# Kernel tuning notes

Hardware: AMD Instinct MI355X
Metric: run time of the kernel (lower is better)

The kernel has to match this reference:

```python
import jax, jax.numpy as jnp
import numpy as np

D_MODEL = 1024
NHEAD = 16
HEAD_DIM = D_MODEL // NHEAD
SF_THRESHOLD = 4.0
SF_LEVELS = 8
SF_STEP = SF_THRESHOLD / SF_LEVELS  # 0.5
EPS = 1e-6


def sfn(x):
    # Scale-and-Fire neuron: quantize activations to multiples of SF_STEP,
    # clipped to +/- num_levels, with straight-through estimator.
    q = jnp.clip(jnp.round(x / SF_STEP), -SF_LEVELS, SF_LEVELS) * SF_STEP
    return x + jax.lax.stop_gradient(q - x)


def qk_norm(x, g):
    # RMS-normalize over the head_dim (last axis) with learnable gain g [Dh].
    rms = jnp.sqrt(jnp.mean(x * x, axis=-1, keepdims=True) + EPS)
    return (x / rms) * g


def setup_inputs() -> dict:
    key = jax.random.key(0)
    ks = jax.random.split(key, 10)
    B, L, D = 2, 2048, D_MODEL
    s = 1.0 / np.sqrt(D)
    return {
        "x": jax.random.normal(ks[0], (B, L, D), dtype=jnp.float32),
        "Wq": jax.random.normal(ks[1], (D, D), dtype=jnp.float32) * s,
        "bq": jnp.zeros((D,), dtype=jnp.float32),
        "Wk": jax.random.normal(ks[2], (D, D), dtype=jnp.float32) * s,
        "bk": jnp.zeros((D,), dtype=jnp.float32),
        "Wv": jax.random.normal(ks[3], (D, D), dtype=jnp.float32) * s,
        "bv": jnp.zeros((D,), dtype=jnp.float32),
        "Wo": jax.random.normal(ks[4], (D, D), dtype=jnp.float32) * s,
        "bo": jnp.zeros((D,), dtype=jnp.float32),
        "gq": jnp.ones((HEAD_DIM,), dtype=jnp.float32),
        "gk": jnp.ones((HEAD_DIM,), dtype=jnp.float32),
    }


def reference(x, Wq, bq, Wk, bk, Wv, bv, Wo, bo, gq, gk):
    B, L, D = x.shape
    H, Dh = NHEAD, HEAD_DIM
    scale = Dh ** (-0.5)

    q = sfn(x @ Wq.T + bq)
    k = sfn(x @ Wk.T + bk)
    v = sfn(x @ Wv.T + bv)

    # [B, L, H, Dh] -> [B, H, L, Dh]
    q = q.reshape(B, L, H, Dh).transpose(0, 2, 1, 3)
    k = k.reshape(B, L, H, Dh).transpose(0, 2, 1, 3)
    v = v.reshape(B, L, H, Dh).transpose(0, 2, 1, 3)

    q = qk_norm(q, gq)
    k = qk_norm(k, gk)

    scores = jnp.einsum('bhqd,bhkd->bhqk', q, k) * scale
    probs = jax.nn.softmax(scores, axis=-1)  # dropout is identity (eval)
    out = jnp.einsum('bhqk,bhkd->bhqd', probs, v)
    out = out.transpose(0, 2, 1, 3).reshape(B, L, D)
    return out @ Wo.T + bo
```

## Files before the change

### kernel.cpp

```cpp
#include <hip/hip_runtime.h>
#include <math.h>


typedef __bf16 bf16;
typedef bf16 bf16x4 __attribute__((ext_vector_type(4)));
typedef bf16 bf16x8 __attribute__((ext_vector_type(8)));
typedef float f32x4 __attribute__((ext_vector_type(4)));
typedef float f32x16 __attribute__((ext_vector_type(16)));
typedef unsigned int u32;
typedef u32 u32x4 __attribute__((ext_vector_type(4)));

#define LOG2E 1.4426950408889634f
#define MFMA16 __builtin_amdgcn_mfma_f32_16x16x32_bf16
#define MFMA32 __builtin_amdgcn_mfma_f32_32x32x16_bf16
#define S_WAITV(N) asm volatile("s_waitcnt vmcnt(" #N ")" ::: "memory")

__device__ __forceinline__ void bar() {
  asm volatile("" ::: "memory");
  __builtin_amdgcn_s_barrier();
  asm volatile("" ::: "memory");
}

__device__ __forceinline__ float sfn_f(float x) {
  return fminf(fmaxf(rintf(x + x), -8.0f), 8.0f) * 0.5f;
}

__device__ __forceinline__ void gload16(const bf16* g, bf16* l) {
  __builtin_amdgcn_global_load_lds((const __attribute__((address_space(1))) void*)g,
                                   (__attribute__((address_space(3))) void*)l, 16, 0, 0);
}

__device__ __forceinline__ u32 pkbf16(float a, float b) {
  unsigned short ua = __builtin_bit_cast(unsigned short, (bf16)a);
  unsigned short ub = __builtin_bit_cast(unsigned short, (bf16)b);
  return (u32)ua | ((u32)ub << 16);
}


__global__ __launch_bounds__(256) void prep_x_kernel(const float* __restrict__ x,
                                                     bf16* __restrict__ ax) {
  int idx = blockIdx.x * 256 + threadIdx.x;
  int m  = idx >> 8;
  int kc = (idx & 255) << 2;
  const float4 v = *(const float4*)(x + (size_t)m * 1024 + kc);
  bf16 h0 = (bf16)v.x, h1 = (bf16)v.y, h2 = (bf16)v.z, h3 = (bf16)v.w;
  bf16 l0 = (bf16)(v.x - (float)h0), l1 = (bf16)(v.y - (float)h1),
       l2 = (bf16)(v.z - (float)h2), l3 = (bf16)(v.w - (float)h3);
  bf16x4 hv = {h0, h1, h2, h3};
  bf16x4 lv = {l0, l1, l2, l3};
  bf16* p = ax + (size_t)m * 3072 + kc;
  *(bf16x4*)(p)        = hv;
  *(bf16x4*)(p + 1024) = lv;
  *(bf16x4*)(p + 2048) = hv;
}

__global__ __launch_bounds__(256) void prep_w_kernel(const float* __restrict__ Wq,
                                                     const float* __restrict__ Wk,
                                                     const float* __restrict__ Wv,
                                                     bf16* __restrict__ wc) {
  int idx = blockIdx.x * 256 + threadIdx.x;
  int mat = idx >> 18;
  int r   = idx & 262143;
  int n   = r >> 8;
  int kc  = (r & 255) << 2;
  const float* W = (mat == 0) ? Wq : ((mat == 1) ? Wk : Wv);
  const float4 v = *(const float4*)(W + (size_t)n * 1024 + kc);
  bf16 h0 = (bf16)v.x, h1 = (bf16)v.y, h2 = (bf16)v.z, h3 = (bf16)v.w;
  bf16 l0 = (bf16)(v.x - (float)h0), l1 = (bf16)(v.y - (float)h1),
       l2 = (bf16)(v.z - (float)h2), l3 = (bf16)(v.w - (float)h3);
  bf16x4 hv = {h0, h1, h2, h3};
  bf16x4 lv = {l0, l1, l2, l3};
  bf16* p = wc + (size_t)(mat * 1024 + n) * 3072 + kc;
  *(bf16x4*)(p)        = hv;
  *(bf16x4*)(p + 1024) = hv;
  *(bf16x4*)(p + 2048) = lv;
}

__global__ __launch_bounds__(256) void prep_wo_kernel(const float* __restrict__ Wo,
                                                      bf16* __restrict__ wob) {
  int idx = blockIdx.x * 256 + threadIdx.x;
  const float4 v = *(const float4*)(Wo + (size_t)idx * 4);
  bf16x4 hv = {(bf16)v.x, (bf16)v.y, (bf16)v.z, (bf16)v.w};
  *(bf16x4*)(wob + (size_t)idx * 4) = hv;
}


__global__ __launch_bounds__(512, 2) void gemm_qkv_kernel(
    const bf16* __restrict__ A, const bf16* __restrict__ Bm,
    const float* __restrict__ b0, const float* __restrict__ b1,
    const float* __restrict__ b2, const float* __restrict__ g0,
    const float* __restrict__ g1, bf16* __restrict__ qn, bf16* __restrict__ kn,
    bf16* __restrict__ vt) {
  constexpr int K = 3072, NT = 48;
  __shared__ bf16 lds[2][28672];
  const int tid  = threadIdx.x;
  const int wave = tid >> 6;
  const int lane = tid & 63;
  const int lm   = lane & 15;
  const int kg   = lane >> 4;
  const int lid     = blockIdx.x;
  const int logical = ((lid & 7) << 5) | (lid >> 3);
  const int m0 = (logical >> 4) << 8;
  const int n0 = (logical & 15) * 192;

  auto stageA = [&](int buf, int half, int kt) {
#pragma unroll
    for (int j = 0; j < 2; ++j) {
      const int c    = j * 512 + tid;
      const int row  = c >> 3;
      const int col8 = (c & 7) ^ (row & 7);
      gload16(A + (size_t)(m0 + half * 128 + row) * K + kt + col8 * 8,
              &lds[buf][half * 8192 + c * 8]);
    }
  };
  auto stageB = [&](int buf, int ch, int kt) {
    const int row  = tid >> 3;
    const int col8 = (tid & 7) ^ (row & 7);
    gload16(Bm + (size_t)(n0 + ch * 64 + row) * K + kt + col8 * 8,
            &lds[buf][16384 + ch * 4096 + tid * 8]);
  };

  const int sw    = lm & 7;
  const int arow  = (wave << 5) + lm;
  auto rdA = [&](int buf, int r, int kk) -> bf16x8 {
    const int row = arow + 16 * r;
    return *(const bf16x8*)&lds[buf][(row >> 7) * 8192 + (row & 127) * 64 +
                                     (((kk << 2) + kg) ^ sw) * 8];
  };
  auto rdB = [&](int buf, int c, int kk) -> bf16x8 {
    const int col = 16 * c + lm;
    return *(const bf16x8*)&lds[buf][16384 + (col >> 6) * 4096 + (col & 63) * 64 +
                                     (((kk << 2) + kg) ^ sw) * 8];
  };

  f32x4 acc[2][12] = {};

  stageA(0, 0, 0); stageA(0, 1, 0);
  stageB(0, 0, 0); stageB(0, 1, 0); stageB(0, 2, 0);
  stageA(1, 0, 64); stageA(1, 1, 64);
  S_WAITV(4);
  bar();

  for (int t = 0; t < NT; ++t) {
    const int cur = t & 1, nxt = cur ^ 1;
    const int kt1 = (t + 1) << 6, kt2 = (t + 2) << 6;
    bf16x8 a[2][2], bv[6];
#pragma unroll
    for (int r = 0; r < 2; ++r)
#pragma unroll
      for (int kk = 0; kk < 2; ++kk)
        a[r][kk] = rdA(cur, r, kk);
#pragma unroll
    for (int c = 0; c < 6; ++c) bv[c] = rdB(cur, c, 0);
    if (t + 1 < NT) stageB(nxt, 0, kt1);
    bar();
    __builtin_amdgcn_s_setprio(1);
#pragma unroll
    for (int r = 0; r < 2; ++r)
#pragma unroll
      for (int c = 0; c < 6; ++c)
        acc[r][c] = MFMA16(a[r][0], bv[c], acc[r][c], 0, 0, 0);
    __builtin_amdgcn_s_setprio(0);
    bar();
    bf16x8 bw[6];
#pragma unroll
    for (int c = 0; c < 6; ++c) bw[c] = rdB(cur, c + 6, 0);
    if (t + 1 < NT) { stageB(nxt, 1, kt1); stageB(nxt, 2, kt1); }
    bar();
    __builtin_amdgcn_s_setprio(1);
#pragma unroll
    for (int r = 0; r < 2; ++r)
#pragma unroll
      for (int c = 0; c < 6; ++c)
        acc[r][c + 6] = MFMA16(a[r][0], bw[c], acc[r][c + 6], 0, 0, 0);
    __builtin_amdgcn_s_setprio(0);
    bar();
    bf16x8 bx[6];
#pragma unroll
    for (int c = 0; c < 6; ++c) bx[c] = rdB(cur, c, 1);
    bar();
    __builtin_amdgcn_s_setprio(1);
#pragma unroll
    for (int r = 0; r < 2; ++r)
#pragma unroll
      for (int c = 0; c < 6; ++c)
        acc[r][c] = MFMA16(a[r][1], bx[c], acc[r][c], 0, 0, 0);
    __builtin_amdgcn_s_setprio(0);
    bar();
    bf16x8 by[6];
#pragma unroll
    for (int c = 0; c < 6; ++c) by[c] = rdB(cur, c + 6, 1);
    if (t + 2 < NT) {
      stageA(cur, 0, kt2); stageA(cur, 1, kt2);
      S_WAITV(4);
    } else {
      S_WAITV(0);
    }
    bar();
    __builtin_amdgcn_s_setprio(1);
#pragma unroll
    for (int r = 0; r < 2; ++r)
#pragma unroll
      for (int c = 0; c < 6; ++c)
        acc[r][c + 6] = MFMA16(a[r][1], by[c], acc[r][c + 6], 0, 0, 0);
    __builtin_amdgcn_s_setprio(0);
    bar();
  }

#pragma unroll
  for (int h = 0; h < 3; ++h) {
    const int gcol = n0 + (h << 6);
    const int mat  = gcol >> 10;
    const int cb   = gcol & 1023;
    const int hh   = cb >> 6;
    const float* bias = (mat == 0) ? b0 : ((mat == 1) ? b1 : b2);
    float bvals[4];
#pragma unroll
    for (int j = 0; j < 4; ++j) bvals[j] = bias[cb + 16 * j + lm];

    if (mat < 2) {
      const float* gain = (mat == 0) ? g0 : g1;
      bf16* dst = (mat == 0) ? qn : kn;
      float gv[4];
#pragma unroll
      for (int j = 0; j < 4; ++j) gv[j] = gain[16 * j + lm];
#pragma unroll
      for (int r = 0; r < 2; ++r) {
        float y[4][4];
        float ss[4] = {0.f, 0.f, 0.f, 0.f};
#pragma unroll
        for (int j = 0; j < 4; ++j)
#pragma unroll
          for (int g = 0; g < 4; ++g) {
            float tq = sfn_f(acc[r][4 * h + j][g] + bvals[j]);
            y[j][g] = tq;
            ss[g] += tq * tq;
          }
#pragma unroll
        for (int g = 0; g < 4; ++g) {
          float s = ss[g];
          s += __shfl_xor(s, 1);
          s += __shfl_xor(s, 2);
          s += __shfl_xor(s, 4);
          s += __shfl_xor(s, 8);
          ss[g] = 1.0f / sqrtf(s * (1.0f / 64.0f) + 1e-6f);
        }
        const int mbase = m0 + (wave << 5) + 16 * r + 4 * kg;
        const int bb = mbase >> 11;
        const int ll = mbase & 2047;
#pragma unroll
        for (int g = 0; g < 4; ++g) {
          bf16* rowp = dst + ((size_t)(bb * 16 + hh) * 2048 + (ll + g)) * 64;
#pragma unroll
          for (int j = 0; j < 4; ++j)
            rowp[16 * j + lm] = (bf16)(y[j][g] * ss[g] * gv[j]);
        }
      }
    } else {
#pragma unroll
      for (int r = 0; r < 2; ++r) {
        const int mbase = m0 + (wave << 5) + 16 * r + 4 * kg;
        const int bb = mbase >> 11;
        const int ll = mbase & 2047;
#pragma unroll
        for (int j = 0; j < 4; ++j) {
          bf16x4 pk;
#pragma unroll
          for (int g = 0; g < 4; ++g)
            pk[g] = (bf16)sfn_f(acc[r][4 * h + j][g] + bvals[j]);
          *(bf16x4*)(vt + ((size_t)(bb * 16 + hh) * 64 + 16 * j + lm) * 2048 + ll) = pk;
        }
      }
    }
  }
}


__global__ __launch_bounds__(256, 3) void gemm_o_kernel(
    const bf16* __restrict__ A, const bf16* __restrict__ Bm, int K,
    const float* __restrict__ b0, float* __restrict__ outf) {
  __shared__ bf16 sA[128 * 32];
  __shared__ bf16 sB[128 * 32];
  const int tid  = threadIdx.x;
  const int wave = tid >> 6;
  const int lane = tid & 63;
  const int lm   = lane & 15;
  const int kg   = lane >> 4;
  const int nbx = gridDim.x;
  const int lid = blockIdx.x + nbx * blockIdx.y;
  const int cpx = (nbx << 5) >> 3;
  const int logical = (lid & 7) * cpx + (lid >> 3);
  const int m0 = (logical / nbx) << 7;
  const int n0 = (logical % nbx) << 7;
  const int wm = (wave >> 1) << 6;
  const int wn = (wave & 1) << 6;

  f32x4 acc[4][4] = {};

  for (int kt = 0; kt < K; kt += 32) {
    __syncthreads();
#pragma unroll
    for (int j = 0; j < 2; ++j) {
      const int i   = wave * 128 + j * 64 + lane;
      const int row = i >> 2;
      const int kc  = (i & 3) << 3;
      gload16(A  + (size_t)(m0 + row) * K + kt + kc, sA + i * 8);
      gload16(Bm + (size_t)(n0 + row) * K + kt + kc, sB + i * 8);
    }
    __syncthreads();
    bf16x8 af[4], bfv[4];
#pragma unroll
    for (int r = 0; r < 4; ++r)
      af[r] = *(const bf16x8*)(sA + (wm + 16 * r + lm) * 32 + kg * 8);
#pragma unroll
    for (int c = 0; c < 4; ++c)
      bfv[c] = *(const bf16x8*)(sB + (wn + 16 * c + lm) * 32 + kg * 8);
#pragma unroll
    for (int r = 0; r < 4; ++r)
#pragma unroll
      for (int c = 0; c < 4; ++c)
        acc[r][c] = MFMA16(af[r], bfv[c], acc[r][c], 0, 0, 0);
  }

  float bvals[4];
#pragma unroll
  for (int c = 0; c < 4; ++c) bvals[c] = b0[n0 + wn + 16 * c + lm];
#pragma unroll
  for (int r = 0; r < 4; ++r) {
    const int mr = m0 + wm + 16 * r + 4 * kg;
#pragma unroll
    for (int c = 0; c < 4; ++c) {
      const int nc = n0 + wn + 16 * c + lm;
#pragma unroll
      for (int g = 0; g < 4; ++g)
        outf[(size_t)(mr + g) * 1024 + nc] = acc[r][c][g] + bvals[c];
    }
  }
}


__global__ __launch_bounds__(256, 2) void attn_kernel(const bf16* __restrict__ qn,
                                                      const bf16* __restrict__ kn,
                                                      const bf16* __restrict__ vt,
                                                      bf16* __restrict__ ao) {
  __shared__ bf16 sK[2][64 * 64];
  __shared__ bf16 sV[2][64 * 64];
  const int tid  = threadIdx.x;
  const int wave = tid >> 6;
  const int lane = tid & 63;
  const int l31  = lane & 31;
  const int hi   = lane >> 5;
  const int lid     = blockIdx.x + (blockIdx.y << 4);
  const int logical = ((lid & 7) << 6) | (lid >> 3);
  const int qblk    = logical & 15;
  const int bh      = logical >> 4;
  const int q0      = (qblk << 7) + (wave << 5);
  const bf16* qb = qn + (size_t)bh * 2048 * 64;
  const bf16* kb = kn + (size_t)bh * 2048 * 64;
  const bf16* vb = vt + (size_t)bh * 64 * 2048;

  const float C1 = 0.125f * LOG2E;
  const float C2 = -8.0f * LOG2E;

  const int srow7 = lane >> 3;
  const int scl   = (lane & 7) ^ srow7;
  auto stageK = [&](int buf, int kt) {
#pragma unroll
    for (int j = 0; j < 2; ++j) {
      const int ci  = wave * 2 + j;
      const int row = ci * 8 + srow7;
      gload16(kb + (size_t)(kt + row) * 64 + scl * 8, &sK[buf][ci * 512]);
    }
  };
  auto stageV = [&](int buf, int kt) {
#pragma unroll
    for (int j = 0; j < 2; ++j) {
      const int ci  = wave * 2 + j;
      const int row = ci * 8 + srow7;
      gload16(vb + (size_t)row * 2048 + kt + scl * 8, &sV[buf][ci * 512]);
    }
  };

  bf16x8 qf[4];
#pragma unroll
  for (int j = 0; j < 4; ++j)
    qf[j] = *(const bf16x8*)(qb + (size_t)(q0 + l31) * 64 + j * 16 + hi * 8);

  f32x16 o[2] = {};
  float lrun = 0.f;

  stageK(0, 0);
  stageV(0, 0);
  S_WAITV(0);
  bar();

  for (int t = 0; t < 32; ++t) {
    const int cur = t & 1;
    if (t < 31) { stageK(cur ^ 1, (t + 1) << 6); stageV(cur ^ 1, (t + 1) << 6); }

#pragma unroll
    for (int ks = 0; ks < 2; ++ks) {
      const int krow = ks * 32 + l31;
      const int ksw  = krow & 7;
      bf16x8 kf[4];
#pragma unroll
      for (int j = 0; j < 4; ++j)
        kf[j] = *(const bf16x8*)(&sK[cur][krow * 64 + ((2 * j + hi) ^ ksw) * 8]);

      f32x16 s = {0.f, 0.f, 0.f, 0.f, 0.f, 0.f, 0.f, 0.f,
                  0.f, 0.f, 0.f, 0.f, 0.f, 0.f, 0.f, 0.f};
      __builtin_amdgcn_s_setprio(1);
#pragma unroll
      for (int j = 0; j < 4; ++j)
        s = MFMA32(kf[j], qf[j], s, 0, 0, 0);
      __builtin_amdgcn_s_setprio(0);

      float p[16];
#pragma unroll
      for (int r = 0; r < 16; ++r) {
        p[r] = __builtin_amdgcn_exp2f(fmaf(s[r], C1, C2));
        lrun += p[r];
      }
      u32 w0 = pkbf16(p[0], p[1]),  w1 = pkbf16(p[2], p[3]);
      u32 w2 = pkbf16(p[4], p[5]),  w3 = pkbf16(p[6], p[7]);
      u32 w4 = pkbf16(p[8], p[9]),  w5 = pkbf16(p[10], p[11]);
      u32 w6 = pkbf16(p[12], p[13]), w7 = pkbf16(p[14], p[15]);
      asm volatile("v_permlane32_swap_b32 %0, %1" : "+v"(w0), "+v"(w2));
      asm volatile("v_permlane32_swap_b32 %0, %1" : "+v"(w1), "+v"(w3));
      asm volatile("v_permlane32_swap_b32 %0, %1" : "+v"(w4), "+v"(w6));
      asm volatile("v_permlane32_swap_b32 %0, %1" : "+v"(w5), "+v"(w7));
      const bf16x8 pb0 = __builtin_bit_cast(bf16x8, (u32x4){w0, w1, w2, w3});
      const bf16x8 pb1 = __builtin_bit_cast(bf16x8, (u32x4){w4, w5, w6, w7});

#pragma unroll
      for (int rb = 0; rb < 2; ++rb) {
        const int vrow = rb * 32 + l31;
        const int vsw  = vrow & 7;
        const bf16x8 vf0 = *(const bf16x8*)(&sV[cur][vrow * 64 + ((4 * ks + hi) ^ vsw) * 8]);
        const bf16x8 vf1 = *(const bf16x8*)(&sV[cur][vrow * 64 + ((4 * ks + 2 + hi) ^ vsw) * 8]);
        __builtin_amdgcn_s_setprio(1);
        o[rb] = MFMA32(vf0, pb0, o[rb], 0, 0, 0);
        o[rb] = MFMA32(vf1, pb1, o[rb], 0, 0, 0);
        __builtin_amdgcn_s_setprio(0);
      }
    }

    S_WAITV(0);
    bar();
  }

  lrun += __shfl_xor(lrun, 32);
  const float inv = 1.0f / lrun;
  const int bb = bh >> 4;
  const int hh = bh & 15;
  bf16* rowp = ao + (size_t)(bb * 2048 + q0 + l31) * 1024 + hh * 64;
#pragma unroll
  for (int rb = 0; rb < 2; ++rb)
#pragma unroll
    for (int r4 = 0; r4 < 4; ++r4) {
      bf16x4 pk;
#pragma unroll
      for (int g = 0; g < 4; ++g)
        pk[g] = (bf16)(o[rb][r4 * 4 + g] * inv);
      *(bf16x4*)(rowp + rb * 32 + r4 * 8 + hi * 4) = pk;
    }
}


extern "C" void kernel_launch(void* const* d_in, const int* in_sizes, int n_in,
                              void* d_out, int out_size, void* d_ws, size_t ws_size,
                              hipStream_t stream) {
  const float* x  = (const float*)d_in[0];
  const float* Wq = (const float*)d_in[1];
  const float* bq = (const float*)d_in[2];
  const float* Wk = (const float*)d_in[3];
  const float* bk = (const float*)d_in[4];
  const float* Wv = (const float*)d_in[5];
  const float* bv = (const float*)d_in[6];
  const float* Wo = (const float*)d_in[7];
  const float* bo = (const float*)d_in[8];
  const float* gq = (const float*)d_in[9];
  const float* gk = (const float*)d_in[10];
  float* out = (float*)d_out;

  char* ws = (char*)d_ws;
  bf16* ax   = (bf16*)(ws);
  bf16* wc   = (bf16*)(ws + 25165824);
  bf16* wob  = (bf16*)(ws + 44040192);
  bf16* qn   = (bf16*)(ws + 46137344);
  bf16* kn   = (bf16*)(ws + 54525952);
  bf16* vt   = (bf16*)(ws + 62914560);
  bf16* attn = (bf16*)(ws + 71303168);

  prep_x_kernel<<<dim3(4096), dim3(256), 0, stream>>>(x, ax);
  prep_w_kernel<<<dim3(3072), dim3(256), 0, stream>>>(Wq, Wk, Wv, wc);
  prep_wo_kernel<<<dim3(1024), dim3(256), 0, stream>>>(Wo, wob);

  gemm_qkv_kernel<<<dim3(256), dim3(512), 0, stream>>>(
      ax, wc, bq, bk, bv, gq, gk, qn, kn, vt);

  attn_kernel<<<dim3(16, 32), dim3(256), 0, stream>>>(qn, kn, vt, attn);

  gemm_o_kernel<<<dim3(8, 32), dim3(256), 0, stream>>>(
      attn, wob, 1024, bo, out);
}
```

Baseline: 252.3 us.

## Retile QKV GEMM waves to 64x96 and pipeline output GEMM with swizzled LDS

```diff
diff --git a/kernel.cpp b/kernel.cpp
--- a/kernel.cpp
+++ b/kernel.cpp
@@ -98,6 +98,8 @@
   const int lane = tid & 63;
   const int lm   = lane & 15;
   const int kg   = lane >> 4;
+  const int wr   = wave & 3;
+  const int wc   = wave >> 2;
   const int lid     = blockIdx.x;
   const int logical = ((lid & 7) << 5) | (lid >> 3);
   const int m0 = (logical >> 4) << 8;
@@ -120,20 +122,18 @@
             &lds[buf][16384 + ch * 4096 + tid * 8]);
   };
 
-  const int sw    = lm & 7;
-  const int arow  = (wave << 5) + lm;
   auto rdA = [&](int buf, int r, int kk) -> bf16x8 {
-    const int row = arow + 16 * r;
+    const int row = (wr << 6) + (r << 4) + lm;
     return *(const bf16x8*)&lds[buf][(row >> 7) * 8192 + (row & 127) * 64 +
-                                     (((kk << 2) + kg) ^ sw) * 8];
+                                     (((kk << 2) + kg) ^ (row & 7)) * 8];
   };
   auto rdB = [&](int buf, int c, int kk) -> bf16x8 {
-    const int col = 16 * c + lm;
+    const int col = wc * 96 + (c << 4) + lm;
     return *(const bf16x8*)&lds[buf][16384 + (col >> 6) * 4096 + (col & 63) * 64 +
-                                     (((kk << 2) + kg) ^ sw) * 8];
-  };
-
-  f32x4 acc[2][12] = {};
+                                     (((kk << 2) + kg) ^ (col & 7)) * 8];
+  };
+
+  f32x4 acc[4][6] = {};
 
   stageA(0, 0, 0); stageA(0, 1, 0);
   stageB(0, 0, 0); stageB(0, 1, 0); stageB(0, 2, 0);
@@ -144,52 +144,48 @@
   for (int t = 0; t < NT; ++t) {
     const int cur = t & 1, nxt = cur ^ 1;
     const int kt1 = (t + 1) << 6, kt2 = (t + 2) << 6;
-    bf16x8 a[2][2], bv[6];
-#pragma unroll
-    for (int r = 0; r < 2; ++r)
-#pragma unroll
-      for (int kk = 0; kk < 2; ++kk)
-        a[r][kk] = rdA(cur, r, kk);
-#pragma unroll
-    for (int c = 0; c < 6; ++c) bv[c] = rdB(cur, c, 0);
+    bf16x8 a0[4], a1[4], bA[3], bB[3], bC[3], bD[3];
+#pragma unroll
+    for (int r = 0; r < 4; ++r) a0[r] = rdA(cur, r, 0);
+#pragma unroll
+    for (int c = 0; c < 3; ++c) bA[c] = rdB(cur, c, 0);
     if (t + 1 < NT) stageB(nxt, 0, kt1);
     bar();
     __builtin_amdgcn_s_setprio(1);
 #pragma unroll
-    for (int r = 0; r < 2; ++r)
-#pragma unroll
-      for (int c = 0; c < 6; ++c)
-        acc[r][c] = MFMA16(a[r][0], bv[c], acc[r][c], 0, 0, 0);
+    for (int r = 0; r < 4; ++r)
+#pragma unroll
+      for (int c = 0; c < 3; ++c)
+        acc[r][c] = MFMA16(a0[r], bA[c], acc[r][c], 0, 0, 0);
     __builtin_amdgcn_s_setprio(0);
     bar();
-    bf16x8 bw[6];
-#pragma unroll
-    for (int c = 0; c < 6; ++c) bw[c] = rdB(cur, c + 6, 0);
+#pragma unroll
+    for (int c = 0; c < 3; ++c) bB[c] = rdB(cur, c + 3, 0);
     if (t + 1 < NT) { stageB(nxt, 1, kt1); stageB(nxt, 2, kt1); }
     bar();
     __builtin_amdgcn_s_setprio(1);
 #pragma unroll
-    for (int r = 0; r < 2; ++r)
-#pragma unroll
-      for (int c = 0; c < 6; ++c)
-        acc[r][c + 6] = MFMA16(a[r][0], bw[c], acc[r][c + 6], 0, 0, 0);
+    for (int r = 0; r < 4; ++r)
+#pragma unroll
+      for (int c = 0; c < 3; ++c)
+        acc[r][c + 3] = MFMA16(a0[r], bB[c], acc[r][c + 3], 0, 0, 0);
     __builtin_amdgcn_s_setprio(0);
     bar();
-    bf16x8 bx[6];
-#pragma unroll
-    for (int c = 0; c < 6; ++c) bx[c] = rdB(cur, c, 1);
+#pragma unroll
+    for (int r = 0; r < 4; ++r) a1[r] = rdA(cur, r, 1);
+#pragma unroll
+    for (int c = 0; c < 3; ++c) bC[c] = rdB(cur, c, 1);
     bar();
     __builtin_amdgcn_s_setprio(1);
 #pragma unroll
-    for (int r = 0; r < 2; ++r)
-#pragma unroll
-      for (int c = 0; c < 6; ++c)
-        acc[r][c] = MFMA16(a[r][1], bx[c], acc[r][c], 0, 0, 0);
+    for (int r = 0; r < 4; ++r)
+#pragma unroll
+      for (int c = 0; c < 3; ++c)
+        acc[r][c] = MFMA16(a1[r], bC[c], acc[r][c], 0, 0, 0);
     __builtin_amdgcn_s_setprio(0);
     bar();
-    bf16x8 by[6];
-#pragma unroll
-    for (int c = 0; c < 6; ++c) by[c] = rdB(cur, c + 6, 1);
+#pragma unroll
+    for (int c = 0; c < 3; ++c) bD[c] = rdB(cur, c + 3, 1);
     if (t + 2 < NT) {
       stageA(cur, 0, kt2); stageA(cur, 1, kt2);
       S_WAITV(4);
@@ -199,138 +195,248 @@
     bar();
     __builtin_amdgcn_s_setprio(1);
 #pragma unroll
-    for (int r = 0; r < 2; ++r)
-#pragma unroll
-      for (int c = 0; c < 6; ++c)
-        acc[r][c + 6] = MFMA16(a[r][1], by[c], acc[r][c + 6], 0, 0, 0);
+    for (int r = 0; r < 4; ++r)
+#pragma unroll
+      for (int c = 0; c < 3; ++c)
+        acc[r][c + 3] = MFMA16(a1[r], bD[c], acc[r][c + 3], 0, 0, 0);
     __builtin_amdgcn_s_setprio(0);
     bar();
   }
 
-#pragma unroll
-  for (int h = 0; h < 3; ++h) {
-    const int gcol = n0 + (h << 6);
-    const int mat  = gcol >> 10;
-    const int cb   = gcol & 1023;
-    const int hh   = cb >> 6;
-    const float* bias = (mat == 0) ? b0 : ((mat == 1) ? b1 : b2);
-    float bvals[4];
-#pragma unroll
-    for (int j = 0; j < 4; ++j) bvals[j] = bias[cb + 16 * j + lm];
-
-    if (mat < 2) {
-      const float* gain = (mat == 0) ? g0 : g1;
-      bf16* dst = (mat == 0) ? qn : kn;
-      float gv[4];
-#pragma unroll
-      for (int j = 0; j < 4; ++j) gv[j] = gain[16 * j + lm];
-#pragma unroll
-      for (int r = 0; r < 2; ++r) {
-        float y[4][4];
-        float ss[4] = {0.f, 0.f, 0.f, 0.f};
-#pragma unroll
-        for (int j = 0; j < 4; ++j)
-#pragma unroll
-          for (int g = 0; g < 4; ++g) {
-            float tq = sfn_f(acc[r][4 * h + j][g] + bvals[j]);
-            y[j][g] = tq;
-            ss[g] += tq * tq;
-          }
-#pragma unroll
-        for (int g = 0; g < 4; ++g) {
-          float s = ss[g];
-          s += __shfl_xor(s, 1);
-          s += __shfl_xor(s, 2);
-          s += __shfl_xor(s, 4);
-          s += __shfl_xor(s, 8);
-          ss[g] = 1.0f / sqrtf(s * (1.0f / 64.0f) + 1e-6f);
-        }
-        const int mbase = m0 + (wave << 5) + 16 * r + 4 * kg;
-        const int bb = mbase >> 11;
-        const int ll = mbase & 2047;
-#pragma unroll
-        for (int g = 0; g < 4; ++g) {
-          bf16* rowp = dst + ((size_t)(bb * 16 + hh) * 2048 + (ll + g)) * 64;
-#pragma unroll
-          for (int j = 0; j < 4; ++j)
-            rowp[16 * j + lm] = (bf16)(y[j][g] * ss[g] * gv[j]);
-        }
-      }
-    } else {
-#pragma unroll
-      for (int r = 0; r < 2; ++r) {
-        const int mbase = m0 + (wave << 5) + 16 * r + 4 * kg;
-        const int bb = mbase >> 11;
-        const int ll = mbase & 2047;
-#pragma unroll
-        for (int j = 0; j < 4; ++j) {
-          bf16x4 pk;
-#pragma unroll
-          for (int g = 0; g < 4; ++g)
-            pk[g] = (bf16)sfn_f(acc[r][4 * h + j][g] + bvals[j]);
-          *(bf16x4*)(vt + ((size_t)(bb * 16 + hh) * 64 + 16 * j + lm) * 2048 + ll) = pk;
-        }
-      }
-    }
+  const int fc0   = wc ? 2 : 0;
+  const int fgcol = n0 + (wc ? 128 : 0);
+  const int hc0   = wc ? 0 : 4;
+  const int hoff  = wc ? 32 : 0;
+  const int hgcol = n0 + 64;
+
+  const int fmat = fgcol >> 10, fhh = (fgcol & 1023) >> 6;
+  const int hmat = hgcol >> 10, hhh = (hgcol & 1023) >> 6;
+  const float* fbias = (fmat == 0) ? b0 : ((fmat == 1) ? b1 : b2);
+  const float* hbias = (hmat == 0) ? b0 : ((hmat == 1) ? b1 : b2);
+
+  float fb[4], hb[2];
+#pragma unroll
+  for (int c = 0; c < 4; ++c) fb[c] = fbias[(fgcol & 1023) + 16 * c + lm];
+#pragma unroll
+  for (int c = 0; c < 2; ++c) hb[c] = hbias[(hgcol & 1023) + hoff + 16 * c + lm];
+
+  float ffs[4][4], phs[4][4];
+#pragma unroll
+  for (int r = 0; r < 4; ++r)
+#pragma unroll
+    for (int g = 0; g < 4; ++g) {
+      float sf = 0.f, sh = 0.f;
+#pragma unroll
+      for (int c = 0; c < 4; ++c) {
+        float t = sfn_f(acc[r][fc0 + c][g] + fb[c]);
+        sf += t * t;
+      }
+#pragma unroll
+      for (int c = 0; c < 2; ++c) {
+        float t = sfn_f(acc[r][hc0 + c][g] + hb[c]);
+        sh += t * t;
+      }
+      ffs[r][g] = sf;
+      phs[r][g] = sh;
+    }
+#pragma unroll
+  for (int r = 0; r < 4; ++r)
+#pragma unroll
+    for (int g = 0; g < 4; ++g)
+#pragma unroll
+      for (int d = 1; d < 16; d <<= 1) {
+        ffs[r][g] += __shfl_xor(ffs[r][g], d);
+        phs[r][g] += __shfl_xor(phs[r][g], d);
+      }
+
+  float* sSS = (float*)&lds[0][0];
+  if (lm == 0) {
+#pragma unroll
+    for (int r = 0; r < 4; ++r)
+#pragma unroll
+      for (int g = 0; g < 4; ++g)
+        sSS[((wr << 1) | wc) * 64 + 16 * r + 4 * kg + g] = phs[r][g];
   }
-}
-
-
-__global__ __launch_bounds__(256, 3) void gemm_o_kernel(
-    const bf16* __restrict__ A, const bf16* __restrict__ Bm, int K,
+  bar();
+  float pot[4][4];
+#pragma unroll
+  for (int r = 0; r < 4; ++r)
+#pragma unroll
+    for (int g = 0; g < 4; ++g)
+      pot[r][g] = sSS[((wr << 1) | (wc ^ 1)) * 64 + 16 * r + 4 * kg + g];
+
+  if (fmat < 2) {
+    const float* gain = (fmat == 0) ? g0 : g1;
+    bf16* dst = (fmat == 0) ? qn : kn;
+    float gv[4];
+#pragma unroll
+    for (int c = 0; c < 4; ++c) gv[c] = gain[16 * c + lm];
+#pragma unroll
+    for (int r = 0; r < 4; ++r) {
+      const int mbase = m0 + (wr << 6) + 16 * r + 4 * kg;
+      const int bb = mbase >> 11;
+      const int ll = mbase & 2047;
+#pragma unroll
+      for (int g = 0; g < 4; ++g) {
+        const float inv = 1.0f / sqrtf(ffs[r][g] * (1.0f / 64.0f) + 1e-6f);
+        bf16* rowp = dst + ((size_t)(bb * 16 + fhh) * 2048 + (ll + g)) * 64;
+#pragma unroll
+        for (int c = 0; c < 4; ++c)
+          rowp[16 * c + lm] = (bf16)(sfn_f(acc[r][fc0 + c][g] + fb[c]) * inv * gv[c]);
+      }
+    }
+  } else {
+#pragma unroll
+    for (int r = 0; r < 4; ++r) {
+      const int mbase = m0 + (wr << 6) + 16 * r + 4 * kg;
+      const int bb = mbase >> 11;
+      const int ll = mbase & 2047;
+#pragma unroll
+      for (int c = 0; c < 4; ++c) {
+        bf16x4 pk;
+#pragma unroll
+        for (int g = 0; g < 4; ++g)
+          pk[g] = (bf16)sfn_f(acc[r][fc0 + c][g] + fb[c]);
+        *(bf16x4*)(vt + ((size_t)(bb * 16 + fhh) * 64 + 16 * c + lm) * 2048 + ll) = pk;
+      }
+    }
+  }
+
+  if (hmat < 2) {
+    const float* gain = (hmat == 0) ? g0 : g1;
+    bf16* dst = (hmat == 0) ? qn : kn;
+    float gv[2];
+#pragma unroll
+    for (int c = 0; c < 2; ++c) gv[c] = gain[hoff + 16 * c + lm];
+#pragma unroll
+    for (int r = 0; r < 4; ++r) {
+      const int mbase = m0 + (wr << 6) + 16 * r + 4 * kg;
+      const int bb = mbase >> 11;
+      const int ll = mbase & 2047;
+#pragma unroll
+      for (int g = 0; g < 4; ++g) {
+        const float ss  = phs[r][g] + pot[r][g];
+        const float inv = 1.0f / sqrtf(ss * (1.0f / 64.0f) + 1e-6f);
+        bf16* rowp = dst + ((size_t)(bb * 16 + hhh) * 2048 + (ll + g)) * 64;
+#pragma unroll
+        for (int c = 0; c < 2; ++c)
+          rowp[hoff + 16 * c + lm] = (bf16)(sfn_f(acc[r][hc0 + c][g] + hb[c]) * inv * gv[c]);
+      }
+    }
+  } else {
+#pragma unroll
+    for (int r = 0; r < 4; ++r) {
+      const int mbase = m0 + (wr << 6) + 16 * r + 4 * kg;
+      const int bb = mbase >> 11;
+      const int ll = mbase & 2047;
+#pragma unroll
+      for (int c = 0; c < 2; ++c) {
+        bf16x4 pk;
+#pragma unroll
+        for (int g = 0; g < 4; ++g)
+          pk[g] = (bf16)sfn_f(acc[r][hc0 + c][g] + hb[c]);
+        *(bf16x4*)(vt + ((size_t)(bb * 16 + hhh) * 64 + hoff + 16 * c + lm) * 2048 + ll) = pk;
+      }
+    }
+  }
+}
+
+
+__global__ __launch_bounds__(256, 2) void gemm_o_kernel(
+    const bf16* __restrict__ A, const bf16* __restrict__ Bm,
     const float* __restrict__ b0, float* __restrict__ outf) {
-  __shared__ bf16 sA[128 * 32];
-  __shared__ bf16 sB[128 * 32];
+  constexpr int K = 1024, NT = 16;
+  __shared__ bf16 lds[2][16384];
   const int tid  = threadIdx.x;
   const int wave = tid >> 6;
   const int lane = tid & 63;
   const int lm   = lane & 15;
   const int kg   = lane >> 4;
-  const int nbx = gridDim.x;
-  const int lid = blockIdx.x + nbx * blockIdx.y;
-  const int cpx = (nbx << 5) >> 3;
-  const int logical = (lid & 7) * cpx + (lid >> 3);
-  const int m0 = (logical / nbx) << 7;
-  const int n0 = (logical % nbx) << 7;
-  const int wm = (wave >> 1) << 6;
-  const int wn = (wave & 1) << 6;
+  const int wr   = wave & 1;
+  const int wcb  = wave >> 1;
+  const int lid     = blockIdx.x;
+  const int logical = ((lid & 7) << 5) | (lid >> 3);
+  const int m0 = (logical >> 3) << 7;
+  const int n0 = (logical & 7) << 7;
+
+  auto stageA = [&](int buf, int kt) {
+#pragma unroll
+    for (int j = 0; j < 4; ++j) {
+      const int i    = j * 256 + tid;
+      const int row  = i >> 3;
+      const int col8 = (i & 7) ^ (row & 7);
+      gload16(A + (size_t)(m0 + row) * K + kt + col8 * 8, &lds[buf][i * 8]);
+    }
+  };
+  auto stageB = [&](int buf, int kt) {
+#pragma unroll
+    for (int j = 0; j < 4; ++j) {
+      const int i    = j * 256 + tid;
+      const int row  = i >> 3;
+      const int col8 = (i & 7) ^ (row & 7);
+      gload16(Bm + (size_t)(n0 + row) * K + kt + col8 * 8, &lds[buf][8192 + i * 8]);
+    }
+  };
+  auto rdA = [&](int buf, int r, int kk) -> bf16x8 {
+    const int row = (wr << 6) + (r << 4) + lm;
+    return *(const bf16x8*)&lds[buf][row * 64 + (((kk << 2) + kg) ^ (row & 7)) * 8];
+  };
+  auto rdB = [&](int buf, int c, int kk) -> bf16x8 {
+    const int row = (wcb << 6) + (c << 4) + lm;
+    return *(const bf16x8*)&lds[buf][8192 + row * 64 + (((kk << 2) + kg) ^ (row & 7)) * 8];
+  };
 
   f32x4 acc[4][4] = {};
 
-  for (int kt = 0; kt < K; kt += 32) {
-    __syncthreads();
-#pragma unroll
-    for (int j = 0; j < 2; ++j) {
-      const int i   = wave * 128 + j * 64 + lane;
-      const int row = i >> 2;
-      const int kc  = (i & 3) << 3;
-      gload16(A  + (size_t)(m0 + row) * K + kt + kc, sA + i * 8);
-      gload16(Bm + (size_t)(n0 + row) * K + kt + kc, sB + i * 8);
-    }
-    __syncthreads();
-    bf16x8 af[4], bfv[4];
+  stageA(0, 0); stageB(0, 0); stageA(1, 64);
+  S_WAITV(4);
+  bar();
+
+  for (int t = 0; t < NT; ++t) {
+    const int cur = t & 1, nxt = cur ^ 1;
+    bf16x8 a0[4], a1[4], bq0[4], bq1[4];
+#pragma unroll
+    for (int r = 0; r < 4; ++r) { a0[r] = rdA(cur, r, 0); a1[r] = rdA(cur, r, 1); }
+#pragma unroll
+    for (int c = 0; c < 4; ++c) bq0[c] = rdB(cur, c, 0);
+    if (t + 1 < NT) stageB(nxt, (t + 1) << 6);
+    bar();
+    __builtin_amdgcn_s_setprio(1);
 #pragma unroll
     for (int r = 0; r < 4; ++r)
-      af[r] = *(const bf16x8*)(sA + (wm + 16 * r + lm) * 32 + kg * 8);
-#pragma unroll
-    for (int c = 0; c < 4; ++c)
-      bfv[c] = *(const bf16x8*)(sB + (wn + 16 * c + lm) * 32 + kg * 8);
+#pragma unroll
+      for (int c = 0; c < 4; ++c)
+        acc[r][c] = MFMA16(a0[r], bq0[c], acc[r][c], 0, 0, 0);
+    __builtin_amdgcn_s_setprio(0);
+    bar();
+#pragma unroll
+    for (int c = 0; c < 4; ++c) bq1[c] = rdB(cur, c, 1);
+    if (t + 2 < NT) {
+      stageA(cur, (t + 2) << 6);
+      S_WAITV(4);
+    } else {
+      S_WAITV(0);
+    }
+    bar();
+    __builtin_amdgcn_s_setprio(1);
 #pragma unroll
     for (int r = 0; r < 4; ++r)
 #pragma unroll
       for (int c = 0; c < 4; ++c)
-        acc[r][c] = MFMA16(af[r], bfv[c], acc[r][c], 0, 0, 0);
+        acc[r][c] = MFMA16(a1[r], bq1[c], acc[r][c], 0, 0, 0);
+    __builtin_amdgcn_s_setprio(0);
+    bar();
   }
 
   float bvals[4];
 #pragma unroll
-  for (int c = 0; c < 4; ++c) bvals[c] = b0[n0 + wn + 16 * c + lm];
+  for (int c = 0; c < 4; ++c) bvals[c] = b0[n0 + (wcb << 6) + 16 * c + lm];
 #pragma unroll
   for (int r = 0; r < 4; ++r) {
-    const int mr = m0 + wm + 16 * r + 4 * kg;
+    const int mr = m0 + (wr << 6) + 16 * r + 4 * kg;
 #pragma unroll
     for (int c = 0; c < 4; ++c) {
-      const int nc = n0 + wn + 16 * c + lm;
+      const int nc = n0 + (wcb << 6) + 16 * c + lm;
 #pragma unroll
       for (int g = 0; g < 4; ++g)
         outf[(size_t)(mr + g) * 1024 + nc] = acc[r][c][g] + bvals[c];
@@ -501,6 +607,5 @@
 
   attn_kernel<<<dim3(16, 32), dim3(256), 0, stream>>>(qn, kn, vt, attn);
 
-  gemm_o_kernel<<<dim3(8, 32), dim3(256), 0, stream>>>(
-      attn, wob, 1024, bo, out);
-}
+  gemm_o_kernel<<<dim3(256), dim3(256), 0, stream>>>(attn, wob, bo, out);
+}
```

After: 245.4 us. -2.7%, faster.
